# Kernel tuning notes

Measured on AMD Instinct MI355X. Metric: run time of the kernel, lower is better.

## Reference

```python
import jax, jax.numpy as jnp
import numpy as np

EPS = 1e-5

def setup_inputs() -> dict:
    key = jax.random.key(0)
    k1, k2 = jax.random.split(key)
    x = jax.random.normal(k1, (4, 2048, 4096), dtype=jnp.float32)
    weight = jax.random.normal(k2, (11008, 4096), dtype=jnp.float32) * 0.02
    return {"x": x, "weight": weight}

def reference(x, weight):
    # scale = mean(|W|) + eps; ternary-quantize W, matmul, rescale output
    scale = jnp.mean(jnp.abs(weight)) + EPS
    Wq = weight / scale                       # [out, in]
    Wt = jnp.clip(jnp.round(Wq), -1.0, 1.0)   # ternary {-1,0,1} (STE adds 0 in value)
    out = jnp.einsum('bsd,od->bso', x, Wt)    # [4,2048,11008]
    return out * scale
```

## Files before the change

kernel.cpp:

```cpp
#include <hip/hip_runtime.h>
#include <hip/hip_bf16.h>
#include <stdint.h>

#define AS1 __attribute__((address_space(1)))
#define AS3 __attribute__((address_space(3)))

typedef __bf16 bf16x8_t __attribute__((ext_vector_type(8)));
typedef __bf16 bf16x4_t __attribute__((ext_vector_type(4)));
typedef float  f32x4_t  __attribute__((ext_vector_type(4)));

constexpr int MD = 8192;
constexpr int ND = 11008;
constexpr int KD = 4096;

constexpr int BM8 = 256, BN8 = 256, BK8 = 64;
constexpr int MT8 = MD / BM8;
constexpr int NT8 = ND / BN8;
constexpr int NWG8 = MT8 * NT8;
constexpr int NKT = KD / BK8;

constexpr int BM = 128, BN = 128, BK = 32;
constexpr int MT = MD / BM, NT = ND / BN, NWG = MT * NT;
constexpr int KSTEPS = KD / BK;

__global__ void k_abs_partial(const float* __restrict__ w, double* __restrict__ part) {
  __shared__ double sm[256];
  const size_t n4 = (size_t)ND * KD / 4;
  const f32x4_t* w4 = (const f32x4_t*)w;
  double s = 0.0;
  for (size_t i = (size_t)blockIdx.x * 256 + threadIdx.x; i < n4; i += (size_t)gridDim.x * 256) {
    f32x4_t v = __builtin_nontemporal_load(&w4[i]);
    s += (double)fabsf(v[0]) + (double)fabsf(v[1]) + (double)fabsf(v[2]) + (double)fabsf(v[3]);
  }
  sm[threadIdx.x] = s;
  __syncthreads();
  for (int o = 128; o > 0; o >>= 1) {
    if ((int)threadIdx.x < o) sm[threadIdx.x] += sm[threadIdx.x + o];
    __syncthreads();
  }
  if (threadIdx.x == 0) part[blockIdx.x] = sm[0];
}

__global__ void k_abs_final(const double* __restrict__ part, float* __restrict__ scale_out) {
  __shared__ double sm[256];
  double s = 0.0;
  for (int i = threadIdx.x; i < 2048; i += 256) s += part[i];
  sm[threadIdx.x] = s;
  __syncthreads();
  for (int o = 128; o > 0; o >>= 1) {
    if ((int)threadIdx.x < o) sm[threadIdx.x] += sm[threadIdx.x + o];
    __syncthreads();
  }
  if (threadIdx.x == 0) {
    double mean = sm[0] / (double)((size_t)ND * KD);
    scale_out[0] = (float)mean + 1e-5f;
  }
}

__global__ void k_quant_w(const float* __restrict__ w, const float* __restrict__ scale_p,
                          __bf16* __restrict__ wq) {
  const float s = scale_p[0];
  const size_t n4 = (size_t)ND * KD / 4;
  const f32x4_t* w4 = (const f32x4_t*)w;
  bf16x4_t* q4 = (bf16x4_t*)wq;
  for (size_t i = (size_t)blockIdx.x * 256 + threadIdx.x; i < n4; i += (size_t)gridDim.x * 256) {
    f32x4_t v = __builtin_nontemporal_load(&w4[i]);
    bf16x4_t h;
#pragma unroll
    for (int j = 0; j < 4; ++j) {
      float q = rintf(v[j] / s);
      q = fminf(1.f, fmaxf(-1.f, q));
      h[j] = (__bf16)q;
    }
    q4[i] = h;
  }
}

__global__ void k_conv_x(const float* __restrict__ x, __bf16* __restrict__ xb) {
  const size_t n4 = (size_t)MD * KD / 4;
  const f32x4_t* x4 = (const f32x4_t*)x;
  bf16x4_t* o4 = (bf16x4_t*)xb;
  for (size_t i = (size_t)blockIdx.x * 256 + threadIdx.x; i < n4; i += (size_t)gridDim.x * 256) {
    f32x4_t v = __builtin_nontemporal_load(&x4[i]);
    bf16x4_t h;
#pragma unroll
    for (int j = 0; j < 4; ++j) h[j] = (__bf16)v[j];
    o4[i] = h;
  }
}


#define BAR8()   __builtin_amdgcn_s_barrier()
#define LGKM0()  asm volatile("s_waitcnt lgkmcnt(0)")
#define LGKM8()  asm volatile("s_waitcnt lgkmcnt(8)")
#define VMC(N)   asm volatile("s_waitcnt vmcnt(" #N ")" ::: "memory")

#define RD_A(BUF, MOFF)                                                          \
  _Pragma("unroll") for (int mm = 0; mm < 4; ++mm) {                             \
    a[mm][0] = *(const bf16x8_t*)(Asl[BUF] + ((MOFF) + mm) * 1024 + aBase + sw0);\
    a[mm][1] = *(const bf16x8_t*)(Asl[BUF] + ((MOFF) + mm) * 1024 + aBase + sw1);\
  }
#define RD_B(BUF, N0)                                                            \
  _Pragma("unroll") for (int nn = 0; nn < 2; ++nn) {                             \
    b[(N0) + nn][0] = *(const bf16x8_t*)(Bsl[BUF] + ((N0) + nn) * 1024 + bBase + sw0); \
    b[(N0) + nn][1] = *(const bf16x8_t*)(Bsl[BUF] + ((N0) + nn) * 1024 + bBase + sw1); \
  }
#define MFMA_Q(MH, NH)                                                           \
  _Pragma("unroll") for (int mm = 0; mm < 4; ++mm)                               \
  _Pragma("unroll") for (int nn = 0; nn < 2; ++nn) {                             \
    f32x4_t& c = acc[(MH) * 4 + mm][(NH) * 2 + nn];                              \
    c = __builtin_amdgcn_mfma_f32_16x16x32_bf16(a[mm][0], b[(NH) * 2 + nn][0], c, 0, 0, 0); \
    c = __builtin_amdgcn_mfma_f32_16x16x32_bf16(a[mm][1], b[(NH) * 2 + nn][1], c, 0, 0, 0); \
  }

#define DO_ITER(T1, T2, T3, FULL)                                                \
                                                                         \
  RD_A(0, 0); RD_B(0, 0);                                                        \
  STAGE(1, 0, 0, (T1));                                                          \
  LGKM8();                                                                       \
  BAR8(); LGKM0();                                                               \
  __builtin_amdgcn_s_setprio(1); MFMA_Q(0, 0); __builtin_amdgcn_s_setprio(0);    \
  BAR8();                                                                        \
                                                                         \
  RD_B(0, 2);                                                                    \
  STAGE(1, 0, 1, (T1));                                                          \
  BAR8(); LGKM0();                                                               \
  __builtin_amdgcn_s_setprio(1); MFMA_Q(0, 1); __builtin_amdgcn_s_setprio(0);    \
  BAR8();                                                                        \
                                                                         \
  RD_A(0, 4);                                                                    \
  if (FULL) STAGE(0, 1, 0, (T2));                                                \
  BAR8(); LGKM0();                                                               \
  __builtin_amdgcn_s_setprio(1); MFMA_Q(1, 0); __builtin_amdgcn_s_setprio(0);    \
  BAR8();                                                                        \
                                                                         \
  if (FULL) STAGE(0, 1, 1, (T2));                                                \
  BAR8(); LGKM0();                                                               \
  __builtin_amdgcn_s_setprio(1); MFMA_Q(1, 1); __builtin_amdgcn_s_setprio(0);    \
  if (FULL) { VMC(4); } else { VMC(0); }                                         \
  BAR8();                                                                        \
                                                                         \
  RD_A(1, 0); RD_B(1, 0);                                                        \
  if (FULL) STAGE(0, 0, 0, (T2));                                                \
  LGKM8();                                                                       \
  BAR8(); LGKM0();                                                               \
  __builtin_amdgcn_s_setprio(1); MFMA_Q(0, 0); __builtin_amdgcn_s_setprio(0);    \
  BAR8();                                                                        \
                                                                         \
  RD_B(1, 2);                                                                    \
  if (FULL) STAGE(0, 0, 1, (T2));                                                \
  BAR8(); LGKM0();                                                               \
  __builtin_amdgcn_s_setprio(1); MFMA_Q(0, 1); __builtin_amdgcn_s_setprio(0);    \
  BAR8();                                                                        \
                                                                         \
  RD_A(1, 4);                                                                    \
  if (FULL) STAGE(1, 1, 0, (T3));                                                \
  BAR8(); LGKM0();                                                               \
  __builtin_amdgcn_s_setprio(1); MFMA_Q(1, 0); __builtin_amdgcn_s_setprio(0);    \
  BAR8();                                                                        \
                                                                         \
  if (FULL) STAGE(1, 1, 1, (T3));                                                \
  BAR8(); LGKM0();                                                               \
  __builtin_amdgcn_s_setprio(1); MFMA_Q(1, 1); __builtin_amdgcn_s_setprio(0);    \
  if (FULL) { VMC(4); }                                                          \
  BAR8();

__global__ __launch_bounds__(512, 2) void k_gemm8(
    const __bf16* __restrict__ xb, const __bf16* __restrict__ wq,
    const float* __restrict__ scale_p, float* __restrict__ out) {
  __shared__ __bf16 smem[2 * 2 * 2 * 8192];

  const int tid  = threadIdx.x;
  const int lane = tid & 63;
  const int wid  = tid >> 6;
  const int wr   = wid >> 2;
  const int wc   = wid & 3;
  const int lr   = lane & 15;
  const int kq   = lane >> 4;

  const int wg = ((int)blockIdx.x & 7) * (NWG8 / 8) + ((int)blockIdx.x >> 3);
  int bm, bn;
  if (wg < 1280) {
    const int g = wg >> 8, r = wg & 255;
    bn = g * 8 + (r & 7);
    bm = r >> 3;
  } else {
    const int r = wg - 1280;
    bn = 40 + r % 3;
    bm = r / 3;
  }

  const float scl = scale_p[0];

  const int c0 = tid, c1 = tid + 512;
  const int r0 = c0 >> 3, q0 = (c0 & 7) ^ (r0 & 7);
  const int r1 = c1 >> 3, q1 = (c1 & 7) ^ (r1 & 7);
  const __bf16* aPan = xb + (size_t)bm * BM8 * KD;
  const __bf16* bPan = wq + (size_t)bn * BN8 * KD;

  auto STAGE = [&](int buf, int op, int half, int tile) {
    const __bf16* pan = op ? bPan : aPan;
    const __bf16* s0 = pan + (size_t)(half * 128 + r0) * KD + tile * 64 + q0 * 8;
    const __bf16* s1 = pan + (size_t)(half * 128 + r1) * KD + tile * 64 + q1 * 8;
    __bf16* d = smem + ((buf * 2 + op) * 2 + half) * 8192;
    __builtin_amdgcn_global_load_lds((AS1 const void*)s0, (AS3 void*)(d + c0 * 8), 16, 0, 0);
    __builtin_amdgcn_global_load_lds((AS1 const void*)s1, (AS3 void*)(d + c1 * 8), 16, 0, 0);
  };

  const int sw0 = ((kq)     ^ (lr & 7)) * 8;
  const int sw1 = ((kq + 4) ^ (lr & 7)) * 8;
  const int aBase = lr * 64;
  const int bBase = ((wc & 1) * 64 + lr) * 64;
  const int bhalf = wc >> 1;
  const __bf16* Asl[2] = { smem + (0 * 4 + 0 * 2 + wr) * 8192,
                           smem + (1 * 4 + 0 * 2 + wr) * 8192 };
  const __bf16* Bsl[2] = { smem + (0 * 4 + 1 * 2 + bhalf) * 8192,
                           smem + (1 * 4 + 1 * 2 + bhalf) * 8192 };

  bf16x8_t a[4][2], b[4][2];
  f32x4_t acc[8][4] = {};

  STAGE(0, 0, 0, 0); STAGE(0, 0, 1, 0);
  STAGE(0, 1, 0, 0); STAGE(0, 1, 1, 0);
  STAGE(1, 1, 0, 1); STAGE(1, 1, 1, 1);
  VMC(4);
  BAR8();

  for (int i = 0; i < 31; ++i) {
    const int t1 = 2 * i + 1, t2 = 2 * i + 2, t3 = 2 * i + 3;
    DO_ITER(t1, t2, t3, 1)
  }
  DO_ITER(63, 0, 0, 0)

  const size_t row0 = (size_t)bm * 256 + wr * 128 + kq * 4;
  const int col0 = bn * 256 + wc * 64 + lr;
#pragma unroll
  for (int m = 0; m < 8; ++m)
#pragma unroll
    for (int j = 0; j < 4; ++j) {
      float* orow = out + (row0 + m * 16 + j) * (size_t)ND + col0;
#pragma unroll
      for (int n = 0; n < 4; ++n)
        __builtin_nontemporal_store(scl * acc[m][n][j], &orow[n * 16]);
    }
}

__global__ void k_gemm_fb(const float* __restrict__ x, const float* __restrict__ w,
                          const float* __restrict__ scale_p, float* __restrict__ out) {
  __shared__ __bf16 As[BM * BK];
  __shared__ __bf16 Bs[BN * BK];

  const int tid  = threadIdx.x;
  const int lane = tid & 63;
  const int wid  = tid >> 6;
  const int wr = wid >> 1, wc = wid & 1;
  const int lr = lane & 15, kq = lane >> 4;

  int wg = ((int)blockIdx.x % 8) * (NWG / 8) + (int)blockIdx.x / 8;
  const int bm = wg % MT;
  const int bn = wg / MT;

  const float scl = scale_p[0];
  const float inv = 1.0f / scl;

  const int c0 = tid, c1 = tid + 256;
  const int r0 = c0 >> 2, kk0 = (c0 & 3) * 8;
  const int r1 = c1 >> 2, kk1 = (c1 & 3) * 8;
  const size_t aBase0 = (size_t)(bm * BM + r0) * KD;
  const size_t aBase1 = (size_t)(bm * BM + r1) * KD;
  const size_t bBase0 = (size_t)(bn * BN + r0) * KD;
  const size_t bBase1 = (size_t)(bn * BN + r1) * KD;

  f32x4_t acc[4][4] = {};

  for (int kt = 0; kt < KSTEPS; ++kt) {
    const int k0 = kt * BK;
    {
      const float* g0 = x + aBase0 + k0 + kk0;
      const float* g1 = x + aBase1 + k0 + kk1;
      f32x4_t v0 = *(const f32x4_t*)g0, v1 = *(const f32x4_t*)(g0 + 4);
      f32x4_t v2 = *(const f32x4_t*)g1, v3 = *(const f32x4_t*)(g1 + 4);
      bf16x8_t h0, h1;
#pragma unroll
      for (int j = 0; j < 4; ++j) {
        h0[j] = (__bf16)v0[j]; h0[j + 4] = (__bf16)v1[j];
        h1[j] = (__bf16)v2[j]; h1[j + 4] = (__bf16)v3[j];
      }
      *(bf16x8_t*)(&As[c0 * 8]) = h0;
      *(bf16x8_t*)(&As[c1 * 8]) = h1;
    }
    {
      const float* g0 = w + bBase0 + k0 + kk0;
      const float* g1 = w + bBase1 + k0 + kk1;
      f32x4_t v0 = *(const f32x4_t*)g0, v1 = *(const f32x4_t*)(g0 + 4);
      f32x4_t v2 = *(const f32x4_t*)g1, v3 = *(const f32x4_t*)(g1 + 4);
      bf16x8_t h0, h1;
#pragma unroll
      for (int j = 0; j < 4; ++j) {
        h0[j]     = (__bf16)fminf(1.f, fmaxf(-1.f, rintf(v0[j] * inv)));
        h0[j + 4] = (__bf16)fminf(1.f, fmaxf(-1.f, rintf(v1[j] * inv)));
        h1[j]     = (__bf16)fminf(1.f, fmaxf(-1.f, rintf(v2[j] * inv)));
        h1[j + 4] = (__bf16)fminf(1.f, fmaxf(-1.f, rintf(v3[j] * inv)));
      }
      *(bf16x8_t*)(&Bs[c0 * 8]) = h0;
      *(bf16x8_t*)(&Bs[c1 * 8]) = h1;
    }
    __syncthreads();
    bf16x8_t a[4], b[4];
#pragma unroll
    for (int m = 0; m < 4; ++m)
      a[m] = *(const bf16x8_t*)(&As[(wr * 64 + m * 16 + lr) * BK + kq * 8]);
#pragma unroll
    for (int n = 0; n < 4; ++n)
      b[n] = *(const bf16x8_t*)(&Bs[(wc * 64 + n * 16 + lr) * BK + kq * 8]);
#pragma unroll
    for (int m = 0; m < 4; ++m)
#pragma unroll
      for (int n = 0; n < 4; ++n)
        acc[m][n] = __builtin_amdgcn_mfma_f32_16x16x32_bf16(a[m], b[n], acc[m][n], 0, 0, 0);
    __syncthreads();
  }

  const size_t row0 = (size_t)bm * BM + wr * 64 + kq * 4;
  const int col0 = bn * BN + wc * 64 + lr;
#pragma unroll
  for (int m = 0; m < 4; ++m)
#pragma unroll
    for (int j = 0; j < 4; ++j) {
      float* orow = out + (row0 + m * 16 + j) * (size_t)ND + col0;
#pragma unroll
      for (int n = 0; n < 4; ++n)
        __builtin_nontemporal_store(scl * acc[m][n][j], &orow[n * 16]);
    }
}

extern "C" void kernel_launch(void* const* d_in, const int* in_sizes, int n_in,
                              void* d_out, int out_size, void* d_ws, size_t ws_size,
                              hipStream_t stream) {
  (void)in_sizes; (void)n_in; (void)out_size;
  const float* x = (const float*)d_in[0];
  const float* w = (const float*)d_in[1];
  float* out = (float*)d_out;

  char* ws = (char*)d_ws;
  float*  scale_p = (float*)ws;
  double* part    = (double*)(ws + 256);
  __bf16* wq      = (__bf16*)(ws + 32768);
  __bf16* xb      = (__bf16*)(ws + 32768 + (size_t)ND * KD * 2);

  const size_t NEED_AB = 32768 + (size_t)ND * KD * 2 + (size_t)MD * KD * 2;
  const bool pre = ws_size >= NEED_AB;

  k_abs_partial<<<2048, 256, 0, stream>>>(w, part);
  k_abs_final<<<1, 256, 0, stream>>>(part, scale_p);

  if (pre) {
    k_quant_w<<<2048, 256, 0, stream>>>(w, scale_p, wq);
    k_conv_x<<<2048, 256, 0, stream>>>(x, xb);
    k_gemm8<<<NWG8, 512, 0, stream>>>(xb, wq, scale_p, out);
  } else {
    k_gemm_fb<<<NWG, 256, 0, stream>>>(x, w, scale_p, out);
  }
}
```

Before: 708.8 us.

## Prefetch next LDS fragments after each MFMA phase and tighten vmcnt waits

Moves the LDS fragment reads for the next MFMA quarter to right after the current quarter's MFMAs, fenced with sched_barrier, so LDS latency overlaps the barrier and the global staging. The first fragment of the next iteration is loaded at the end of the previous one, with a prologue read added before the loop. The vmcnt waits move one phase earlier with a lower count (2 instead of 4). This restructures the software pipeline; register pressure and the correctness of the buffer hazards depend on the barrier placement.

```diff
diff --git a/kernel.cpp b/kernel.cpp
--- a/kernel.cpp
+++ b/kernel.cpp
@@ -17,7 +17,6 @@
 constexpr int MT8 = MD / BM8;
 constexpr int NT8 = ND / BN8;
 constexpr int NWG8 = MT8 * NT8;
-constexpr int NKT = KD / BK8;
 
 constexpr int BM = 128, BN = 128, BK = 32;
 constexpr int MT = MD / BM, NT = ND / BN, NWG = MT * NT;
@@ -90,10 +89,10 @@
 }
 
 
-#define BAR8()   __builtin_amdgcn_s_barrier()
-#define LGKM0()  asm volatile("s_waitcnt lgkmcnt(0)")
-#define LGKM8()  asm volatile("s_waitcnt lgkmcnt(8)")
-#define VMC(N)   asm volatile("s_waitcnt vmcnt(" #N ")" ::: "memory")
+#define BAR8()    __builtin_amdgcn_s_barrier()
+#define LGKMC(N)  asm volatile("s_waitcnt lgkmcnt(" #N ")")
+#define VMC(N)    asm volatile("s_waitcnt vmcnt(" #N ")" ::: "memory")
+#define SCHB()    __builtin_amdgcn_sched_barrier(0)
 
 #define RD_A(BUF, MOFF)                                                          \
   _Pragma("unroll") for (int mm = 0; mm < 4; ++mm) {                             \
@@ -114,55 +113,53 @@
   }
 
 #define DO_ITER(T1, T2, T3, FULL)                                                \
-                                                                         \
-  RD_A(0, 0); RD_B(0, 0);                                                        \
+                          \
   STAGE(1, 0, 0, (T1));                                                          \
-  LGKM8();                                                                       \
-  BAR8(); LGKM0();                                                               \
+  BAR8(); LGKMC(0);                                                              \
   __builtin_amdgcn_s_setprio(1); MFMA_Q(0, 0); __builtin_amdgcn_s_setprio(0);    \
-  BAR8();                                                                        \
-                                                                         \
-  RD_B(0, 2);                                                                    \
+  SCHB(); RD_B(0, 2); SCHB();                                     \
+  BAR8();                                                                        \
+                                                       \
   STAGE(1, 0, 1, (T1));                                                          \
-  BAR8(); LGKM0();                                                               \
+  BAR8(); LGKMC(0);                                                              \
   __builtin_amdgcn_s_setprio(1); MFMA_Q(0, 1); __builtin_amdgcn_s_setprio(0);    \
-  BAR8();                                                                        \
-                                                                         \
-  RD_A(0, 4);                                                                    \
+  SCHB(); RD_A(0, 4); SCHB();                     \
+  BAR8();                                                                        \
+                          \
   if (FULL) STAGE(0, 1, 0, (T2));                                                \
-  BAR8(); LGKM0();                                                               \
+  BAR8(); LGKMC(0);                                                              \
   __builtin_amdgcn_s_setprio(1); MFMA_Q(1, 0); __builtin_amdgcn_s_setprio(0);    \
-  BAR8();                                                                        \
-                                                                         \
+  if (FULL) { VMC(2); } else { VMC(0); }                                         \
+  BAR8();                                                                        \
+        \
   if (FULL) STAGE(0, 1, 1, (T2));                                                \
-  BAR8(); LGKM0();                                                               \
+  BAR8();                                                                        \
   __builtin_amdgcn_s_setprio(1); MFMA_Q(1, 1); __builtin_amdgcn_s_setprio(0);    \
-  if (FULL) { VMC(4); } else { VMC(0); }                                         \
-  BAR8();                                                                        \
-                                                                         \
-  RD_A(1, 0); RD_B(1, 0);                                                        \
+  SCHB(); RD_A(1, 0); RD_B(1, 0); SCHB();                                        \
+  BAR8();                                                                        \
+                                                            \
   if (FULL) STAGE(0, 0, 0, (T2));                                                \
-  LGKM8();                                                                       \
-  BAR8(); LGKM0();                                                               \
+  BAR8(); LGKMC(0);                                                              \
   __builtin_amdgcn_s_setprio(1); MFMA_Q(0, 0); __builtin_amdgcn_s_setprio(0);    \
-  BAR8();                                                                        \
-                                                                         \
-  RD_B(1, 2);                                                                    \
+  SCHB(); RD_B(1, 2); SCHB();                                     \
+  BAR8();                                                                        \
+                                                            \
   if (FULL) STAGE(0, 0, 1, (T2));                                                \
-  BAR8(); LGKM0();                                                               \
+  BAR8(); LGKMC(0);                                                              \
   __builtin_amdgcn_s_setprio(1); MFMA_Q(0, 1); __builtin_amdgcn_s_setprio(0);    \
-  BAR8();                                                                        \
-                                                                         \
-  RD_A(1, 4);                                                                    \
+  SCHB(); RD_A(1, 4); SCHB();                                     \
+  BAR8();                                                                        \
+                              \
   if (FULL) STAGE(1, 1, 0, (T3));                                                \
-  BAR8(); LGKM0();                                                               \
+  BAR8(); LGKMC(0);                                                              \
   __builtin_amdgcn_s_setprio(1); MFMA_Q(1, 0); __builtin_amdgcn_s_setprio(0);    \
-  BAR8();                                                                        \
-                                                                         \
+  if (FULL) { VMC(2); }                                                          \
+  BAR8();                                                                        \
+           \
   if (FULL) STAGE(1, 1, 1, (T3));                                                \
-  BAR8(); LGKM0();                                                               \
+  BAR8();                                                                        \
   __builtin_amdgcn_s_setprio(1); MFMA_Q(1, 1); __builtin_amdgcn_s_setprio(0);    \
-  if (FULL) { VMC(4); }                                                          \
+  if (FULL) { SCHB(); RD_A(0, 0); RD_B(0, 0); SCHB(); }                          \
   BAR8();
 
 __global__ __launch_bounds__(512, 2) void k_gemm8(
@@ -225,6 +222,7 @@
   STAGE(1, 1, 0, 1); STAGE(1, 1, 1, 1);
   VMC(4);
   BAR8();
+  SCHB(); RD_A(0, 0); RD_B(0, 0); SCHB();
 
   for (int i = 0; i < 31; ++i) {
     const int t1 = 2 * i + 1, t2 = 2 * i + 2, t3 = 2 * i + 3;
```

Measured after the change: 707.0 us. About the same (-0.3%).
